# Performance work log

Hardware: AMD Instinct MI355X
Metric: run time of the kernel (lower is better)

The kernel has to match this reference:

```python
import jax, jax.numpy as jnp
import numpy as np

B, N, C_IN, C_OUT = 32, 4096, 16, 64
EMB, LINK, WIN = 16, 3, 12


def setup_inputs() -> dict:
    key = jax.random.key(0)
    ks = jax.random.split(key, 7)
    s = lambda k, shape, sc=1.0: jax.random.normal(k, shape, dtype=jnp.float32) * sc
    return {
        "x": s(ks[0], (B, N, C_IN)),
        "x_window": s(ks[1], (B, WIN, N, C_IN)),
        "node_embeddings": s(ks[2], (N, EMB)),
        "weights_pool": s(ks[3], (EMB, LINK, C_IN, C_OUT), 0.1),
        "weights_window": s(ks[4], (EMB, C_IN, C_OUT), 0.1),
        "bias_pool": s(ks[5], (EMB, C_OUT), 0.1),
        "T": s(ks[6], (WIN,), 0.1),
    }


def reference(x, x_window, node_embeddings, weights_pool, weights_window, bias_pool, T):
    # Adaptive adjacency: softmax over rows of relu(E E^T)   [N, N]
    n = node_embeddings.shape[0]
    supports = jax.nn.softmax(
        jax.nn.relu(node_embeddings @ node_embeddings.T), axis=1)
    # Chebyshev polynomial hops: T0=I, T1=A, Tk = 2*A*T(k-1) - T(k-2)
    support_set = [jnp.eye(n, dtype=supports.dtype), supports]
    for _ in range(2, weights_pool.shape[1]):
        support_set.append(2.0 * (supports @ support_set[-1]) - support_set[-2])
    supports_k = jnp.stack(support_set, axis=0)  # [K, N, N]

    # Per-node weight generation from node embeddings
    weights = jnp.einsum('nd,dkio->nkio', node_embeddings, weights_pool)  # [N,K,Cin,Cout]
    bias = node_embeddings @ bias_pool  # [N, Cout]

    # Multi-hop spatial graph convolution
    x_g = jnp.einsum('knm,bmc->bnkc', supports_k, x)  # [B, N, K, Cin]
    x_gconv = jnp.einsum('bnki,nkio->bno', x_g, weights) + bias  # [B, N, Cout]

    # Temporal window transformation: time-mix with T, per-node weights
    x_w = jnp.einsum('btni,t->bni', x_window, T)  # [B, N, Cin]
    w_win = jnp.einsum('nd,dio->nio', node_embeddings, weights_window)  # [N,Cin,Cout]
    x_wconv = jnp.einsum('bni,nio->bno', x_w, w_win)  # [B, N, Cout]

    return x_gconv + x_wconv
```

## Files before the change

kernel.cpp:

```cpp
#include <hip/hip_runtime.h>
#include <hip/hip_bf16.h>

#define NN 4096
#define BB 32
#define CIN 16
#define COUT 64
#define EMB 16
#define KLINK 3
#define WWIN 12
#define BCIN (BB * CIN)
#define KSPLIT 4
#define KCHUNK (NN / KSPLIT)
#define NT (KCHUNK / 32)

typedef unsigned short ushort_t;
typedef __attribute__((ext_vector_type(8))) short bf16x8;
typedef __attribute__((ext_vector_type(4))) float f32x4;
typedef __attribute__((ext_vector_type(4))) unsigned short us4;
typedef __attribute__((ext_vector_type(8))) unsigned short us8;

static __device__ __forceinline__ ushort_t f2bf(float f) {
  union { float f; unsigned u; } v; v.f = f;
  const unsigned r = v.u + 0x7fffu + ((v.u >> 16) & 1u);
  return (ushort_t)(r >> 16);
}

__device__ __forceinline__ void gload16(const void* g, void* l) {
  __builtin_amdgcn_global_load_lds(
      (const __attribute__((address_space(1))) void*)g,
      (__attribute__((address_space(3))) void*)l, 16, 0, 0);
}

__global__ __launch_bounds__(256) void prep_kernel(
    const float* __restrict__ E, const float* __restrict__ Wp,
    const float* __restrict__ Wwp, const float* __restrict__ biasp,
    ushort_t* __restrict__ Ebf, ushort_t* __restrict__ Wpct,
    float* __restrict__ biasn, float* __restrict__ r) {
  const int gid = blockIdx.x * 256 + threadIdx.x;
  if (gid < NN) {
    r[gid] = 0.0f;
    const float* e = E + (size_t)gid * EMB;
    ushort_t* o = Ebf + (size_t)gid * 32;
    #pragma unroll
    for (int d = 0; d < 16; ++d) o[d] = f2bf(e[d]);
    #pragma unroll
    for (int d = 16; d < 32; ++d) o[d] = 0;
  } else if (gid < 2 * NN) {
    const int j = gid - NN;
    const int oo = j >> 6;
    const int i = j & 63;
    const int q = i >> 4;
    const int ii = i & 15;
    ushort_t* w = Wpct + (size_t)j * 32;
    #pragma unroll
    for (int d = 0; d < 16; ++d) {
      float v;
      if (q == 0)
        v = Wp[((size_t)(d * 3 + 0) * 16 + ii) * 64 + oo] -
            Wp[((size_t)(d * 3 + 2) * 16 + ii) * 64 + oo];
      else if (q == 1)
        v = Wp[((size_t)(d * 3 + 1) * 16 + ii) * 64 + oo];
      else if (q == 2)
        v = 2.0f * Wp[((size_t)(d * 3 + 2) * 16 + ii) * 64 + oo];
      else
        v = Wwp[((size_t)d * 16 + ii) * 64 + oo];
      w[d] = f2bf(v);
    }
    #pragma unroll
    for (int d = 16; d < 32; ++d) w[d] = 0;
  } else {
    const int t = gid - 2 * NN;
    if (t < NN * 16) {
      const int n = t >> 4;
      const int o4 = t & 15;
      const float4* bp4 = reinterpret_cast<const float4*>(biasp);
      float4 acc = make_float4(0.f, 0.f, 0.f, 0.f);
      #pragma unroll
      for (int d = 0; d < 16; ++d) {
        const float e = E[(size_t)n * EMB + d];
        const float4 b = bp4[d * 16 + o4];
        acc.x += e * b.x; acc.y += e * b.y; acc.z += e * b.z; acc.w += e * b.w;
      }
      *reinterpret_cast<float4*>(biasn + (size_t)n * 64 + o4 * 4) = acc;
    }
  }
}

__global__ __launch_bounds__(256) void mix_kernel(
    const float* __restrict__ x, const float* __restrict__ xw,
    const float* __restrict__ Tv,
    ushort_t* __restrict__ XtT, float* __restrict__ XW) {
  __shared__ ushort_t T[16][72];
  const int bid = blockIdx.x;
  const int tid = threadIdx.x;
  if (bid < 1024) {
    const int lin = bid * 256 + tid;
    const int c4 = (lin & 3) << 2;
    const int nn0 = ((lin >> 6) & 127) * 32 + ((lin >> 2) & 15);
    const int b = lin >> 13;
    float tv[WWIN];
    #pragma unroll
    for (int t = 0; t < WWIN; ++t) tv[t] = Tv[t];
    float4 a0 = make_float4(0.f, 0.f, 0.f, 0.f);
    float4 a1 = make_float4(0.f, 0.f, 0.f, 0.f);
    #pragma unroll 3
    for (int t = 0; t < WWIN; ++t) {
      const float4 v0 = *reinterpret_cast<const float4*>(
          xw + (((size_t)b * WWIN + t) * NN + nn0) * CIN + c4);
      const float4 v1 = *reinterpret_cast<const float4*>(
          xw + (((size_t)b * WWIN + t) * NN + nn0 + 16) * CIN + c4);
      a0.x += v0.x * tv[t]; a0.y += v0.y * tv[t];
      a0.z += v0.z * tv[t]; a0.w += v0.w * tv[t];
      a1.x += v1.x * tv[t]; a1.y += v1.y * tv[t];
      a1.z += v1.z * tv[t]; a1.w += v1.w * tv[t];
    }
    *reinterpret_cast<float4*>(XW + ((size_t)b * NN + nn0) * CIN + c4) = a0;
    *reinterpret_cast<float4*>(XW + ((size_t)b * NN + nn0 + 16) * CIN + c4) = a1;
  } else {
    const int bx = bid - 1024;
    const int b = bx >> 6;
    const int m0 = (bx & 63) * 64;
    const int i = tid & 15;
    const int ml = tid >> 4;
    #pragma unroll
    for (int it = 0; it < 4; ++it) {
      const int m = m0 + ml + it * 16;
      T[i][ml + it * 16] = f2bf(x[((size_t)b * NN + m) * CIN + i]);
    }
    __syncthreads();
    if (tid < 128) {
      const int rr = tid >> 3;
      const int c8 = (tid & 7) * 8;
      const us8 v = *reinterpret_cast<const us8*>(&T[rr][c8]);
      *reinterpret_cast<us8*>(&XtT[(size_t)(b * CIN + rr) * NN + m0 + c8]) = v;
    }
  }
}

__global__ __launch_bounds__(256) void gemm_mfma_kernel(
    const ushort_t* __restrict__ Ag, const ushort_t* __restrict__ Bt,
    ushort_t* __restrict__ Ct, int lda, int ldb, int ldc, int Kdim) {
  __shared__ ushort_t As[128 * 32];
  __shared__ ushort_t Bs[64 * 32];
  const int tid = threadIdx.x;
  const int lane = tid & 63;
  const int wid = tid >> 6;
  const int wr = wid >> 1;
  const int wc = wid & 1;
  const int row0 = blockIdx.y * 128;
  const int col0 = blockIdx.x * 64;

  f32x4 acc[4][2];
  #pragma unroll
  for (int i = 0; i < 4; ++i)
    #pragma unroll
    for (int j = 0; j < 2; ++j) acc[i][j] = (f32x4){0.f, 0.f, 0.f, 0.f};

  const int sr = tid >> 2;
  const int scs = (((tid & 3) ^ (sr & 3)) * 8);
  const ushort_t* agp0 = Ag + (size_t)(row0 + sr) * lda + scs;
  const ushort_t* agp1 = Ag + (size_t)(row0 + 64 + sr) * lda + scs;
  const ushort_t* bgp  = Bt + (size_t)(col0 + sr) * ldb + scs;
  ushort_t* asl0 = &As[tid * 8];
  ushort_t* asl1 = &As[2048 + tid * 8];
  ushort_t* bsl  = &Bs[tid * 8];

  const int kq = (lane >> 4) * 8;
  const int fr = lane & 15;

  for (int kb = 0; kb < Kdim; kb += 32) {
    gload16(agp0 + kb, asl0);
    gload16(agp1 + kb, asl1);
    gload16(bgp + kb, bsl);
    __syncthreads();

    bf16x8 af[4], bfr[2];
    #pragma unroll
    for (int i = 0; i < 4; ++i) {
      const int r = wr * 64 + i * 16 + fr;
      af[i] = *reinterpret_cast<const bf16x8*>(&As[r * 32 + (kq ^ ((r & 3) * 8))]);
    }
    #pragma unroll
    for (int j = 0; j < 2; ++j) {
      const int r = wc * 32 + j * 16 + fr;
      bfr[j] = *reinterpret_cast<const bf16x8*>(&Bs[r * 32 + (kq ^ ((r & 3) * 8))]);
    }
    #pragma unroll
    for (int i = 0; i < 4; ++i)
      #pragma unroll
      for (int j = 0; j < 2; ++j)
        acc[i][j] = __builtin_amdgcn_mfma_f32_16x16x32_bf16(af[i], bfr[j],
                                                            acc[i][j], 0, 0, 0);
    __syncthreads();
  }

  #pragma unroll
  for (int i = 0; i < 4; ++i) {
    const int rg = row0 + wr * 64 + i * 16 + ((lane >> 4) << 2);
    #pragma unroll
    for (int j = 0; j < 2; ++j) {
      const int cg = col0 + wc * 32 + j * 16 + (lane & 15);
      us4 o;
      o.x = f2bf(acc[i][j][0]);
      o.y = f2bf(acc[i][j][1]);
      o.z = f2bf(acc[i][j][2]);
      o.w = f2bf(acc[i][j][3]);
      *reinterpret_cast<us4*>(&Ct[(size_t)cg * ldc + rg]) = o;
    }
  }
}

template <int CUR>
__device__ __forceinline__ void compute_tile(
    const ushort_t (&As)[3][128 * 32], const ushort_t (&Bs)[3][64 * 32],
    f32x4 (&acc)[4][2], int wr, int wc, int kq, int fr) {
  bf16x8 af[4], bfr[2];
  #pragma unroll
  for (int i = 0; i < 4; ++i) {
    const int rr = wr * 64 + i * 16 + fr;
    af[i] = *reinterpret_cast<const bf16x8*>(
        &As[CUR][rr * 32 + (kq ^ ((rr & 3) * 8))]);
  }
  #pragma unroll
  for (int j = 0; j < 2; ++j) {
    const int rr = wc * 32 + j * 16 + fr;
    bfr[j] = *reinterpret_cast<const bf16x8*>(
        &Bs[CUR][rr * 32 + (kq ^ ((rr & 3) * 8))]);
  }
  #pragma unroll
  for (int i = 0; i < 4; ++i)
    #pragma unroll
    for (int j = 0; j < 2; ++j)
      acc[i][j] = __builtin_amdgcn_mfma_f32_16x16x32_bf16(af[i], bfr[j],
                                                          acc[i][j], 0, 0, 0);
}

__global__ __launch_bounds__(256) void gemm_splitk_kernel(
    const ushort_t* __restrict__ Ag, const ushort_t* __restrict__ Bt,
    float* __restrict__ Cp, int lda, int ldb, int ldc) {
  __shared__ ushort_t As[3][128 * 32];
  __shared__ ushort_t Bs[3][64 * 32];
  const int tid = threadIdx.x;
  const int lane = tid & 63;
  const int wid = tid >> 6;
  const int wr = wid >> 1;
  const int wc = wid & 1;

  const int gx = gridDim.x, gy = gridDim.y;
  const int nwg = gx * gy * gridDim.z;
  int L = blockIdx.x + gx * (blockIdx.y + gy * blockIdx.z);
  L = (L & 7) * (nwg >> 3) + (L >> 3);
  const int bx = L % gx;
  const int by = (L / gx) % gy;
  const int bz = L / (gx * gy);

  const int row0 = by * 128;
  const int col0 = bx * 64;
  const int kbase = bz * KCHUNK;

  f32x4 acc[4][2];
  #pragma unroll
  for (int i = 0; i < 4; ++i)
    #pragma unroll
    for (int j = 0; j < 2; ++j) acc[i][j] = (f32x4){0.f, 0.f, 0.f, 0.f};

  const int sr = tid >> 2;
  const int scs = (((tid & 3) ^ (sr & 3)) * 8);
  const ushort_t* agp0 = Ag + (size_t)(row0 + sr) * lda + scs;
  const ushort_t* agp1 = Ag + (size_t)(row0 + 64 + sr) * lda + scs;
  const ushort_t* bgp  = Bt + (size_t)(col0 + sr) * ldb + scs;

  const int kq = (lane >> 4) * 8;
  const int fr = lane & 15;

#define STAGE(BUF, KB)                              \
  gload16(agp0 + (KB), &As[BUF][tid * 8]);          \
  gload16(agp1 + (KB), &As[BUF][2048 + tid * 8]);   \
  gload16(bgp + (KB), &Bs[BUF][tid * 8]);

#define PIPE_STEP(CUR, NB, TT)                                  \
  STAGE(NB, kbase + ((TT) + 2) * 32);                           \
  asm volatile("s_waitcnt vmcnt(6)" ::: "memory");              \
  __builtin_amdgcn_s_barrier();                                 \
  __builtin_amdgcn_sched_barrier(0);                            \
  compute_tile<CUR>(As, Bs, acc, wr, wc, kq, fr);               \
  __builtin_amdgcn_sched_barrier(0);                            \
  __builtin_amdgcn_s_barrier();

  STAGE(0, kbase);
  STAGE(1, kbase + 32);

  for (int tt = 0; tt < (NT - 2) / 3; ++tt) {
    const int t3 = tt * 3;
    PIPE_STEP(0, 2, t3 + 0);
    PIPE_STEP(1, 0, t3 + 1);
    PIPE_STEP(2, 1, t3 + 2);
  }
  asm volatile("s_waitcnt vmcnt(3)" ::: "memory");
  __builtin_amdgcn_s_barrier();
  __builtin_amdgcn_sched_barrier(0);
  compute_tile<0>(As, Bs, acc, wr, wc, kq, fr);
  __builtin_amdgcn_sched_barrier(0);
  __builtin_amdgcn_s_barrier();
  asm volatile("s_waitcnt vmcnt(0)" ::: "memory");
  __builtin_amdgcn_s_barrier();
  __builtin_amdgcn_sched_barrier(0);
  compute_tile<1>(As, Bs, acc, wr, wc, kq, fr);

#undef PIPE_STEP
#undef STAGE

  float* cpz = Cp + (size_t)bz * ((size_t)BCIN * NN);
  #pragma unroll
  for (int i = 0; i < 4; ++i) {
    const int rg = row0 + wr * 64 + i * 16 + ((lane >> 4) << 2);
    #pragma unroll
    for (int j = 0; j < 2; ++j) {
      const int cg = col0 + wc * 32 + j * 16 + (lane & 15);
      *reinterpret_cast<f32x4*>(&cpz[(size_t)cg * ldc + rg]) = acc[i][j];
    }
  }
}

__global__ __launch_bounds__(256) void reduce_y1_kernel(
    const float* __restrict__ Cp, const float* __restrict__ R,
    ushort_t* __restrict__ Y1T, ushort_t* __restrict__ Y1n) {
  __shared__ ushort_t T[64][72];
  const int n0 = blockIdx.x * 64;
  const int bc0 = blockIdx.y * 64;
  const int tid = threadIdx.x;
  const size_t SS = (size_t)BCIN * NN;
  #pragma unroll
  for (int q = 0; q < 4; ++q) {
    const int lin = tid + q * 256;
    const int bc = lin >> 4;
    const int nc = (lin & 15) * 4;
    const size_t base = (size_t)(bc0 + bc) * NN + n0 + nc;
    float4 s = *reinterpret_cast<const float4*>(Cp + base);
    #pragma unroll
    for (int z = 1; z < KSPLIT; ++z) {
      const float4 v = *reinterpret_cast<const float4*>(Cp + (size_t)z * SS + base);
      s.x += v.x; s.y += v.y; s.z += v.z; s.w += v.w;
    }
    const float4 rv = *reinterpret_cast<const float4*>(R + n0 + nc);
    us4 o;
    o.x = f2bf(s.x / rv.x); o.y = f2bf(s.y / rv.y);
    o.z = f2bf(s.z / rv.z); o.w = f2bf(s.w / rv.w);
    *reinterpret_cast<us4*>(&Y1T[base]) = o;
    *reinterpret_cast<us4*>(&T[bc][nc]) = o;
  }
  __syncthreads();
  #pragma unroll
  for (int t = 0; t < 2; ++t) {
    const int lin = tid + t * 256;
    const int nr = lin >> 3;
    const int ch = lin & 7;
    us8 v;
    #pragma unroll
    for (int e = 0; e < 8; ++e) v[e] = T[ch * 8 + e][nr];
    *reinterpret_cast<us8*>(&Y1n[(size_t)(n0 + nr) * BCIN + bc0 + ch * 8]) = v;
  }
}

__global__ __launch_bounds__(256) void reduce_y2_kernel(
    const float* __restrict__ Cp, ushort_t* __restrict__ Ct,
    const float* __restrict__ R) {
  const size_t e = ((size_t)blockIdx.x * 256 + threadIdx.x) << 2;
  const size_t SS = (size_t)BCIN * NN;
  float4 s = *reinterpret_cast<const float4*>(Cp + e);
  #pragma unroll
  for (int z = 1; z < KSPLIT; ++z) {
    const float4 v = *reinterpret_cast<const float4*>(Cp + (size_t)z * SS + e);
    s.x += v.x; s.y += v.y; s.z += v.z; s.w += v.w;
  }
  const float ri = 1.0f / R[e >> 9];
  s.x *= ri; s.y *= ri; s.z *= ri; s.w *= ri;
  us4 o;
  o.x = f2bf(s.x); o.y = f2bf(s.y); o.z = f2bf(s.z); o.w = f2bf(s.w);
  *reinterpret_cast<us4*>(Ct + e) = o;
}

__global__ __launch_bounds__(256) void pgemm_kernel(
    const ushort_t* __restrict__ Ebf, ushort_t* __restrict__ Pb,
    float* __restrict__ r) {
  __shared__ ushort_t As[128 * 32];
  __shared__ ushort_t Bs[64 * 32];
  const int tid = threadIdx.x;
  const int lane = tid & 63;
  const int wid = tid >> 6;
  const int wr = wid >> 1;
  const int wc = wid & 1;
  const int row0 = blockIdx.y * 128;
  const int col0 = blockIdx.x * 64;

  const int sr = tid >> 2;
  const int scs = (((tid & 3) ^ (sr & 3)) * 8);
  gload16(Ebf + (size_t)(row0 + sr) * 32 + scs, &As[tid * 8]);
  gload16(Ebf + (size_t)(row0 + 64 + sr) * 32 + scs, &As[2048 + tid * 8]);
  gload16(Ebf + (size_t)(col0 + sr) * 32 + scs, &Bs[tid * 8]);
  __syncthreads();

  const int kq = (lane >> 4) * 8;
  const int fr = lane & 15;
  bf16x8 af[4], bfr[2];
  #pragma unroll
  for (int i = 0; i < 4; ++i) {
    const int rr = wr * 64 + i * 16 + fr;
    af[i] = *reinterpret_cast<const bf16x8*>(&As[rr * 32 + (kq ^ ((rr & 3) * 8))]);
  }
  #pragma unroll
  for (int j = 0; j < 2; ++j) {
    const int rr = wc * 32 + j * 16 + fr;
    bfr[j] = *reinterpret_cast<const bf16x8*>(&Bs[rr * 32 + (kq ^ ((rr & 3) * 8))]);
  }
  f32x4 acc[4][2];
  #pragma unroll
  for (int i = 0; i < 4; ++i)
    #pragma unroll
    for (int j = 0; j < 2; ++j) acc[i][j] = (f32x4){0.f, 0.f, 0.f, 0.f};
  #pragma unroll
  for (int i = 0; i < 4; ++i)
    #pragma unroll
    for (int j = 0; j < 2; ++j)
      acc[i][j] = __builtin_amdgcn_mfma_f32_16x16x32_bf16(af[i], bfr[j],
                                                          acc[i][j], 0, 0, 0);

  float pv[4][2][4];
  #pragma unroll
  for (int i = 0; i < 4; ++i) {
    const int rg = row0 + wr * 64 + i * 16 + ((lane >> 4) << 2);
    #pragma unroll
    for (int j = 0; j < 2; ++j) {
      const int cg = col0 + wc * 32 + j * 16 + (lane & 15);
      us4 o;
      #pragma unroll
      for (int q = 0; q < 4; ++q) {
        const float p = __expf(fmaxf(acc[i][j][q], 0.0f) - 16.0f);
        pv[i][j][q] = p;
        o[q] = f2bf(p);
      }
      *reinterpret_cast<us4*>(&Pb[(size_t)cg * NN + rg]) = o;
    }
  }
  #pragma unroll
  for (int i = 0; i < 4; ++i) {
    const int rg = row0 + wr * 64 + i * 16 + ((lane >> 4) << 2);
    #pragma unroll
    for (int q = 0; q < 4; ++q) {
      float s = pv[i][0][q] + pv[i][1][q];
      s += __shfl_xor(s, 1, 64);
      s += __shfl_xor(s, 2, 64);
      s += __shfl_xor(s, 4, 64);
      s += __shfl_xor(s, 8, 64);
      if ((lane & 15) == 0) atomicAdd(&r[rg + q], s);
    }
  }
}

__global__ __launch_bounds__(256) void combine_kernel(
    const float* __restrict__ x, const ushort_t* __restrict__ Y1n,
    const ushort_t* __restrict__ Y2n, const float* __restrict__ XW,
    const ushort_t* __restrict__ Wall, const float* __restrict__ biasn,
    float* __restrict__ out) {
  __shared__ ushort_t lds[4 * 6144];
  const int tid = threadIdx.x;
  const int lane = tid & 63;
  const int w = tid >> 6;
  ushort_t* Wl = lds + w * 6144;
  ushort_t* Vl = Wl + 4096;

  const int perm = ((lane >> 3) << 3) | ((lane & 7) ^ (lane >> 3));
  const int vb = lane >> 1;
  const int i0 = (lane & 1) * 8;

  for (int it = 0; it < 2; ++it) {
    const int n = blockIdx.x * 8 + w * 2 + it;
    asm volatile("s_waitcnt lgkmcnt(0)" ::: "memory");

    const ushort_t* wrow = Wall + (size_t)n * 4096;
    #pragma unroll
    for (int q = 0; q < 8; ++q)
      gload16(wrow + q * 512 + perm * 8, Wl + q * 512);

    const float4* xp = reinterpret_cast<const float4*>(
        x + ((size_t)vb * NN + n) * CIN + i0);
    const float4 xa = xp[0], xb = xp[1];
    const us8 y1 = *reinterpret_cast<const us8*>(Y1n + (size_t)n * BCIN + lane * 8);
    const us8 y2 = *reinterpret_cast<const us8*>(Y2n + (size_t)n * BCIN + lane * 8);
    const float4* xwp = reinterpret_cast<const float4*>(
        XW + ((size_t)vb * NN + n) * CIN + i0);
    const float4 wa = xwp[0], wb = xwp[1];
    us8 xv, wv;
    xv[0] = f2bf(xa.x); xv[1] = f2bf(xa.y); xv[2] = f2bf(xa.z); xv[3] = f2bf(xa.w);
    xv[4] = f2bf(xb.x); xv[5] = f2bf(xb.y); xv[6] = f2bf(xb.z); xv[7] = f2bf(xb.w);
    wv[0] = f2bf(wa.x); wv[1] = f2bf(wa.y); wv[2] = f2bf(wa.z); wv[3] = f2bf(wa.w);
    wv[4] = f2bf(wb.x); wv[5] = f2bf(wb.y); wv[6] = f2bf(wb.z); wv[7] = f2bf(wb.w);
    const int c0 = (lane & 1);
    const int vswz = vb & 7;
    *reinterpret_cast<us8*>(Vl + vb * 64 + (((c0 + 0) ^ vswz) << 3)) = xv;
    *reinterpret_cast<us8*>(Vl + vb * 64 + (((c0 + 2) ^ vswz) << 3)) = y1;
    *reinterpret_cast<us8*>(Vl + vb * 64 + (((c0 + 4) ^ vswz) << 3)) = y2;
    *reinterpret_cast<us8*>(Vl + vb * 64 + (((c0 + 6) ^ vswz) << 3)) = wv;

    f32x4 acc[2][4];
    #pragma unroll
    for (int nt = 0; nt < 4; ++nt) {
      const float bv = biasn[(size_t)n * 64 + nt * 16 + (lane & 15)];
      acc[0][nt] = (f32x4){bv, bv, bv, bv};
      acc[1][nt] = (f32x4){bv, bv, bv, bv};
    }

    asm volatile("s_waitcnt vmcnt(0)" ::: "memory");

    bf16x8 af[2][2], bfr[4][2];
    #pragma unroll
    for (int mt = 0; mt < 2; ++mt)
      #pragma unroll
      for (int kt = 0; kt < 2; ++kt) {
        const int rr = mt * 16 + (lane & 15);
        const int c = kt * 4 + (lane >> 4);
        af[mt][kt] = *reinterpret_cast<const bf16x8*>(
            Vl + rr * 64 + ((c ^ (lane & 7)) << 3));
      }
    #pragma unroll
    for (int nt = 0; nt < 4; ++nt)
      #pragma unroll
      for (int kt = 0; kt < 2; ++kt) {
        const int o = nt * 16 + (lane & 15);
        const int c = kt * 4 + (lane >> 4);
        bfr[nt][kt] = *reinterpret_cast<const bf16x8*>(
            Wl + o * 64 + ((c ^ (lane & 7)) << 3));
      }
    #pragma unroll
    for (int mt = 0; mt < 2; ++mt)
      #pragma unroll
      for (int nt = 0; nt < 4; ++nt)
        #pragma unroll
        for (int kt = 0; kt < 2; ++kt)
          acc[mt][nt] = __builtin_amdgcn_mfma_f32_16x16x32_bf16(
              af[mt][kt], bfr[nt][kt], acc[mt][nt], 0, 0, 0);

    #pragma unroll
    for (int mt = 0; mt < 2; ++mt)
      #pragma unroll
      for (int nt = 0; nt < 4; ++nt) {
        const int o = nt * 16 + (lane & 15);
        #pragma unroll
        for (int rr = 0; rr < 4; ++rr) {
          const int b = mt * 16 + ((lane >> 4) << 2) + rr;
          out[((size_t)b * NN + n) * COUT + o] = acc[mt][nt][rr];
        }
      }
  }
}

extern "C" void kernel_launch(void* const* d_in, const int* in_sizes, int n_in,
                              void* d_out, int out_size, void* d_ws,
                              size_t ws_size, hipStream_t stream) {
  const float* x = (const float*)d_in[0];
  const float* x_window = (const float*)d_in[1];
  const float* E = (const float*)d_in[2];
  const float* Wp = (const float*)d_in[3];
  const float* Wwp = (const float*)d_in[4];
  const float* biasp = (const float*)d_in[5];
  const float* Tv = (const float*)d_in[6];
  float* out = (float*)d_out;

  char* p = (char*)d_ws;
  float* XW = (float*)p;                 p += (size_t)BB * NN * CIN * 4;
  ushort_t* Pb = (ushort_t*)p;           p += (size_t)NN * NN * 2;
  ushort_t* XtT = (ushort_t*)p;          p += (size_t)BCIN * NN * 2;
  ushort_t* Y1T = (ushort_t*)p;          p += (size_t)BCIN * NN * 2;
  ushort_t* Y2n = (ushort_t*)p;          p += (size_t)NN * BCIN * 2;
  ushort_t* Y1n = (ushort_t*)p;          p += (size_t)NN * BCIN * 2;
  ushort_t* Wall = (ushort_t*)p;         p += (size_t)NN * 4096 * 2;
  ushort_t* Ebf = (ushort_t*)p;          p += (size_t)NN * 32 * 2;
  ushort_t* Wpct = (ushort_t*)p;         p += (size_t)NN * 32 * 2;
  float* biasn = (float*)p;              p += (size_t)NN * 64 * 4;
  float* r = (float*)p;                  p += (size_t)NN * 4;
  float* Cpart = (float*)p;              p += (size_t)KSPLIT * BCIN * NN * 4;

  prep_kernel<<<288, 256, 0, stream>>>(E, Wp, Wwp, biasp, Ebf, Wpct, biasn, r);
  gemm_mfma_kernel<<<dim3(NN / 64, NN / 128), 256, 0, stream>>>(
      Wpct, Ebf, Wall, 32, 32, NN, 32);
  pgemm_kernel<<<dim3(NN / 64, NN / 128), 256, 0, stream>>>(Ebf, Pb, r);
  mix_kernel<<<3072, 256, 0, stream>>>(x, x_window, Tv, XtT, XW);
  gemm_splitk_kernel<<<dim3(BCIN / 64, NN / 128, KSPLIT), 256, 0, stream>>>(
      Pb, XtT, Cpart, NN, NN, NN);
  reduce_y1_kernel<<<dim3(NN / 64, BCIN / 64), 256, 0, stream>>>(
      Cpart, r, Y1T, Y1n);
  gemm_splitk_kernel<<<dim3(NN / 64, BCIN / 128, KSPLIT), 256, 0, stream>>>(
      Y1T, Pb, Cpart, NN, NN, BCIN);
  reduce_y2_kernel<<<(BCIN * NN / 4) / 256, 256, 0, stream>>>(Cpart, Y2n, r);
  combine_kernel<<<NN / 8, 256, 0, stream>>>(x, Y1n, Y2n, XW, Wall, biasn, out);
}
```

Before: 192.8 us.

## Merge weight GEMM, P GEMM and mix kernels into one interleaved launch

Three independent kernels (the per-node weight GEMM, the exp(relu(EE^T)) GEMM with row sums, and the time-mix/transpose kernel) are merged into a single uber_kernel. Work types are interleaved by block index in groups of 14, so compute-heavy MFMA tiles and bandwidth-heavy mix blocks share the GPU at the same time. This removes two launch gaps and the tail-end idling between them. The cost is a larger shared-memory footprint per block, set by the biggest role, which may lower occupancy for the lighter roles.

New measurement: 180.4 us. 6.4% less time.

```diff
diff --git a/kernel.cpp b/kernel.cpp
--- a/kernel.cpp
+++ b/kernel.cpp
@@ -86,15 +86,148 @@
   }
 }
 
-__global__ __launch_bounds__(256) void mix_kernel(
+__global__ __launch_bounds__(256) void uber_kernel(
+    const ushort_t* __restrict__ Ebf, const ushort_t* __restrict__ Wpct,
+    ushort_t* __restrict__ Wall, ushort_t* __restrict__ Pb,
+    float* __restrict__ r,
     const float* __restrict__ x, const float* __restrict__ xw,
     const float* __restrict__ Tv,
     ushort_t* __restrict__ XtT, float* __restrict__ XW) {
-  __shared__ ushort_t T[16][72];
+  __shared__ ushort_t smem[6144];
   const int bid = blockIdx.x;
   const int tid = threadIdx.x;
-  if (bid < 1024) {
-    const int lin = bid * 256 + tid;
+  const int g = bid / 14;
+  const int rm = bid - g * 14;
+
+  if (rm < 4) {
+    const int pidx = g * 4 + rm;
+    const int row0 = (pidx >> 6) * 128;
+    const int col0 = (pidx & 63) * 64;
+    ushort_t* As = smem;
+    ushort_t* Bs = smem + 4096;
+    const int lane = tid & 63;
+    const int wid = tid >> 6;
+    const int wr = wid >> 1;
+    const int wc = wid & 1;
+    const int sr = tid >> 2;
+    const int scs = (((tid & 3) ^ (sr & 3)) * 8);
+    gload16(Ebf + (size_t)(row0 + sr) * 32 + scs, &As[tid * 8]);
+    gload16(Ebf + (size_t)(row0 + 64 + sr) * 32 + scs, &As[2048 + tid * 8]);
+    gload16(Ebf + (size_t)(col0 + sr) * 32 + scs, &Bs[tid * 8]);
+    __syncthreads();
+
+    const int kq = (lane >> 4) * 8;
+    const int fr = lane & 15;
+    bf16x8 af[4], bfr[2];
+    #pragma unroll
+    for (int i = 0; i < 4; ++i) {
+      const int rr = wr * 64 + i * 16 + fr;
+      af[i] = *reinterpret_cast<const bf16x8*>(&As[rr * 32 + (kq ^ ((rr & 3) * 8))]);
+    }
+    #pragma unroll
+    for (int j = 0; j < 2; ++j) {
+      const int rr = wc * 32 + j * 16 + fr;
+      bfr[j] = *reinterpret_cast<const bf16x8*>(&Bs[rr * 32 + (kq ^ ((rr & 3) * 8))]);
+    }
+    f32x4 acc[4][2];
+    #pragma unroll
+    for (int i = 0; i < 4; ++i)
+      #pragma unroll
+      for (int j = 0; j < 2; ++j) acc[i][j] = (f32x4){0.f, 0.f, 0.f, 0.f};
+    #pragma unroll
+    for (int i = 0; i < 4; ++i)
+      #pragma unroll
+      for (int j = 0; j < 2; ++j)
+        acc[i][j] = __builtin_amdgcn_mfma_f32_16x16x32_bf16(af[i], bfr[j],
+                                                            acc[i][j], 0, 0, 0);
+    float pv[4][2][4];
+    #pragma unroll
+    for (int i = 0; i < 4; ++i) {
+      const int rg = row0 + wr * 64 + i * 16 + ((lane >> 4) << 2);
+      #pragma unroll
+      for (int j = 0; j < 2; ++j) {
+        const int cg = col0 + wc * 32 + j * 16 + (lane & 15);
+        us4 o;
+        #pragma unroll
+        for (int q = 0; q < 4; ++q) {
+          const float p = __expf(fmaxf(acc[i][j][q], 0.0f) - 16.0f);
+          pv[i][j][q] = p;
+          o[q] = f2bf(p);
+        }
+        *reinterpret_cast<us4*>(&Pb[(size_t)cg * NN + rg]) = o;
+      }
+    }
+    #pragma unroll
+    for (int i = 0; i < 4; ++i) {
+      const int rg = row0 + wr * 64 + i * 16 + ((lane >> 4) << 2);
+      #pragma unroll
+      for (int q = 0; q < 4; ++q) {
+        float s = pv[i][0][q] + pv[i][1][q];
+        s += __shfl_xor(s, 1, 64);
+        s += __shfl_xor(s, 2, 64);
+        s += __shfl_xor(s, 4, 64);
+        s += __shfl_xor(s, 8, 64);
+        if ((lane & 15) == 0) atomicAdd(&r[rg + q], s);
+      }
+    }
+  } else if (rm < 8) {
+    const int widx = g * 4 + (rm - 4);
+    const int row0 = (widx >> 6) * 128;
+    const int col0 = (widx & 63) * 64;
+    ushort_t* As = smem;
+    ushort_t* Bs = smem + 4096;
+    const int lane = tid & 63;
+    const int wid = tid >> 6;
+    const int wr = wid >> 1;
+    const int wc = wid & 1;
+    const int sr = tid >> 2;
+    const int scs = (((tid & 3) ^ (sr & 3)) * 8);
+    gload16(Wpct + (size_t)(row0 + sr) * 32 + scs, &As[tid * 8]);
+    gload16(Wpct + (size_t)(row0 + 64 + sr) * 32 + scs, &As[2048 + tid * 8]);
+    gload16(Ebf + (size_t)(col0 + sr) * 32 + scs, &Bs[tid * 8]);
+    __syncthreads();
+
+    const int kq = (lane >> 4) * 8;
+    const int fr = lane & 15;
+    bf16x8 af[4], bfr[2];
+    #pragma unroll
+    for (int i = 0; i < 4; ++i) {
+      const int rr = wr * 64 + i * 16 + fr;
+      af[i] = *reinterpret_cast<const bf16x8*>(&As[rr * 32 + (kq ^ ((rr & 3) * 8))]);
+    }
+    #pragma unroll
+    for (int j = 0; j < 2; ++j) {
+      const int rr = wc * 32 + j * 16 + fr;
+      bfr[j] = *reinterpret_cast<const bf16x8*>(&Bs[rr * 32 + (kq ^ ((rr & 3) * 8))]);
+    }
+    f32x4 acc[4][2];
+    #pragma unroll
+    for (int i = 0; i < 4; ++i)
+      #pragma unroll
+      for (int j = 0; j < 2; ++j) acc[i][j] = (f32x4){0.f, 0.f, 0.f, 0.f};
+    #pragma unroll
+    for (int i = 0; i < 4; ++i)
+      #pragma unroll
+      for (int j = 0; j < 2; ++j)
+        acc[i][j] = __builtin_amdgcn_mfma_f32_16x16x32_bf16(af[i], bfr[j],
+                                                            acc[i][j], 0, 0, 0);
+    #pragma unroll
+    for (int i = 0; i < 4; ++i) {
+      const int rg = row0 + wr * 64 + i * 16 + ((lane >> 4) << 2);
+      #pragma unroll
+      for (int j = 0; j < 2; ++j) {
+        const int cg = col0 + wc * 32 + j * 16 + (lane & 15);
+        us4 o;
+        o.x = f2bf(acc[i][j][0]);
+        o.y = f2bf(acc[i][j][1]);
+        o.z = f2bf(acc[i][j][2]);
+        o.w = f2bf(acc[i][j][3]);
+        *reinterpret_cast<us4*>(&Wall[(size_t)cg * NN + rg]) = o;
+      }
+    }
+  } else if (rm < 10) {
+    const int tidx = g * 2 + (rm - 8);
+    const int lin = tidx * 256 + tid;
     const int c4 = (lin & 3) << 2;
     const int nn0 = ((lin >> 6) & 127) * 32 + ((lin >> 2) & 15);
     const int b = lin >> 13;
@@ -117,9 +250,10 @@
     *reinterpret_cast<float4*>(XW + ((size_t)b * NN + nn0) * CIN + c4) = a0;
     *reinterpret_cast<float4*>(XW + ((size_t)b * NN + nn0 + 16) * CIN + c4) = a1;
   } else {
-    const int bx = bid - 1024;
-    const int b = bx >> 6;
-    const int m0 = (bx & 63) * 64;
+    const int txidx = g * 4 + (rm - 10);
+    const int b = txidx >> 6;
+    const int m0 = (txidx & 63) * 64;
+    ushort_t (*T)[72] = reinterpret_cast<ushort_t(*)[72]>(smem);
     const int i = tid & 15;
     const int ml = tid >> 4;
     #pragma unroll
@@ -133,79 +267,6 @@
       const int c8 = (tid & 7) * 8;
       const us8 v = *reinterpret_cast<const us8*>(&T[rr][c8]);
       *reinterpret_cast<us8*>(&XtT[(size_t)(b * CIN + rr) * NN + m0 + c8]) = v;
-    }
-  }
-}
-
-__global__ __launch_bounds__(256) void gemm_mfma_kernel(
-    const ushort_t* __restrict__ Ag, const ushort_t* __restrict__ Bt,
-    ushort_t* __restrict__ Ct, int lda, int ldb, int ldc, int Kdim) {
-  __shared__ ushort_t As[128 * 32];
-  __shared__ ushort_t Bs[64 * 32];
-  const int tid = threadIdx.x;
-  const int lane = tid & 63;
-  const int wid = tid >> 6;
-  const int wr = wid >> 1;
-  const int wc = wid & 1;
-  const int row0 = blockIdx.y * 128;
-  const int col0 = blockIdx.x * 64;
-
-  f32x4 acc[4][2];
-  #pragma unroll
-  for (int i = 0; i < 4; ++i)
-    #pragma unroll
-    for (int j = 0; j < 2; ++j) acc[i][j] = (f32x4){0.f, 0.f, 0.f, 0.f};
-
-  const int sr = tid >> 2;
-  const int scs = (((tid & 3) ^ (sr & 3)) * 8);
-  const ushort_t* agp0 = Ag + (size_t)(row0 + sr) * lda + scs;
-  const ushort_t* agp1 = Ag + (size_t)(row0 + 64 + sr) * lda + scs;
-  const ushort_t* bgp  = Bt + (size_t)(col0 + sr) * ldb + scs;
-  ushort_t* asl0 = &As[tid * 8];
-  ushort_t* asl1 = &As[2048 + tid * 8];
-  ushort_t* bsl  = &Bs[tid * 8];
-
-  const int kq = (lane >> 4) * 8;
-  const int fr = lane & 15;
-
-  for (int kb = 0; kb < Kdim; kb += 32) {
-    gload16(agp0 + kb, asl0);
-    gload16(agp1 + kb, asl1);
-    gload16(bgp + kb, bsl);
-    __syncthreads();
-
-    bf16x8 af[4], bfr[2];
-    #pragma unroll
-    for (int i = 0; i < 4; ++i) {
-      const int r = wr * 64 + i * 16 + fr;
-      af[i] = *reinterpret_cast<const bf16x8*>(&As[r * 32 + (kq ^ ((r & 3) * 8))]);
-    }
-    #pragma unroll
-    for (int j = 0; j < 2; ++j) {
-      const int r = wc * 32 + j * 16 + fr;
-      bfr[j] = *reinterpret_cast<const bf16x8*>(&Bs[r * 32 + (kq ^ ((r & 3) * 8))]);
-    }
-    #pragma unroll
-    for (int i = 0; i < 4; ++i)
-      #pragma unroll
-      for (int j = 0; j < 2; ++j)
-        acc[i][j] = __builtin_amdgcn_mfma_f32_16x16x32_bf16(af[i], bfr[j],
-                                                            acc[i][j], 0, 0, 0);
-    __syncthreads();
-  }
-
-  #pragma unroll
-  for (int i = 0; i < 4; ++i) {
-    const int rg = row0 + wr * 64 + i * 16 + ((lane >> 4) << 2);
-    #pragma unroll
-    for (int j = 0; j < 2; ++j) {
-      const int cg = col0 + wc * 32 + j * 16 + (lane & 15);
-      us4 o;
-      o.x = f2bf(acc[i][j][0]);
-      o.y = f2bf(acc[i][j][1]);
-      o.z = f2bf(acc[i][j][2]);
-      o.w = f2bf(acc[i][j][3]);
-      *reinterpret_cast<us4*>(&Ct[(size_t)cg * ldc + rg]) = o;
     }
   }
 }
@@ -378,83 +439,6 @@
   us4 o;
   o.x = f2bf(s.x); o.y = f2bf(s.y); o.z = f2bf(s.z); o.w = f2bf(s.w);
   *reinterpret_cast<us4*>(Ct + e) = o;
-}
-
-__global__ __launch_bounds__(256) void pgemm_kernel(
-    const ushort_t* __restrict__ Ebf, ushort_t* __restrict__ Pb,
-    float* __restrict__ r) {
-  __shared__ ushort_t As[128 * 32];
-  __shared__ ushort_t Bs[64 * 32];
-  const int tid = threadIdx.x;
-  const int lane = tid & 63;
-  const int wid = tid >> 6;
-  const int wr = wid >> 1;
-  const int wc = wid & 1;
-  const int row0 = blockIdx.y * 128;
-  const int col0 = blockIdx.x * 64;
-
-  const int sr = tid >> 2;
-  const int scs = (((tid & 3) ^ (sr & 3)) * 8);
-  gload16(Ebf + (size_t)(row0 + sr) * 32 + scs, &As[tid * 8]);
-  gload16(Ebf + (size_t)(row0 + 64 + sr) * 32 + scs, &As[2048 + tid * 8]);
-  gload16(Ebf + (size_t)(col0 + sr) * 32 + scs, &Bs[tid * 8]);
-  __syncthreads();
-
-  const int kq = (lane >> 4) * 8;
-  const int fr = lane & 15;
-  bf16x8 af[4], bfr[2];
-  #pragma unroll
-  for (int i = 0; i < 4; ++i) {
-    const int rr = wr * 64 + i * 16 + fr;
-    af[i] = *reinterpret_cast<const bf16x8*>(&As[rr * 32 + (kq ^ ((rr & 3) * 8))]);
-  }
-  #pragma unroll
-  for (int j = 0; j < 2; ++j) {
-    const int rr = wc * 32 + j * 16 + fr;
-    bfr[j] = *reinterpret_cast<const bf16x8*>(&Bs[rr * 32 + (kq ^ ((rr & 3) * 8))]);
-  }
-  f32x4 acc[4][2];
-  #pragma unroll
-  for (int i = 0; i < 4; ++i)
-    #pragma unroll
-    for (int j = 0; j < 2; ++j) acc[i][j] = (f32x4){0.f, 0.f, 0.f, 0.f};
-  #pragma unroll
-  for (int i = 0; i < 4; ++i)
-    #pragma unroll
-    for (int j = 0; j < 2; ++j)
-      acc[i][j] = __builtin_amdgcn_mfma_f32_16x16x32_bf16(af[i], bfr[j],
-                                                          acc[i][j], 0, 0, 0);
-
-  float pv[4][2][4];
-  #pragma unroll
-  for (int i = 0; i < 4; ++i) {
-    const int rg = row0 + wr * 64 + i * 16 + ((lane >> 4) << 2);
-    #pragma unroll
-    for (int j = 0; j < 2; ++j) {
-      const int cg = col0 + wc * 32 + j * 16 + (lane & 15);
-      us4 o;
-      #pragma unroll
-      for (int q = 0; q < 4; ++q) {
-        const float p = __expf(fmaxf(acc[i][j][q], 0.0f) - 16.0f);
-        pv[i][j][q] = p;
-        o[q] = f2bf(p);
-      }
-      *reinterpret_cast<us4*>(&Pb[(size_t)cg * NN + rg]) = o;
-    }
-  }
-  #pragma unroll
-  for (int i = 0; i < 4; ++i) {
-    const int rg = row0 + wr * 64 + i * 16 + ((lane >> 4) << 2);
-    #pragma unroll
-    for (int q = 0; q < 4; ++q) {
-      float s = pv[i][0][q] + pv[i][1][q];
-      s += __shfl_xor(s, 1, 64);
-      s += __shfl_xor(s, 2, 64);
-      s += __shfl_xor(s, 4, 64);
-      s += __shfl_xor(s, 8, 64);
-      if ((lane & 15) == 0) atomicAdd(&r[rg + q], s);
-    }
-  }
 }
 
 __global__ __launch_bounds__(256) void combine_kernel(
@@ -581,10 +565,8 @@
   float* Cpart = (float*)p;              p += (size_t)KSPLIT * BCIN * NN * 4;
 
   prep_kernel<<<288, 256, 0, stream>>>(E, Wp, Wwp, biasp, Ebf, Wpct, biasn, r);
-  gemm_mfma_kernel<<<dim3(NN / 64, NN / 128), 256, 0, stream>>>(
-      Wpct, Ebf, Wall, 32, 32, NN, 32);
-  pgemm_kernel<<<dim3(NN / 64, NN / 128), 256, 0, stream>>>(Ebf, Pb, r);
-  mix_kernel<<<3072, 256, 0, stream>>>(x, x_window, Tv, XtT, XW);
+  uber_kernel<<<7168, 256, 0, stream>>>(Ebf, Wpct, Wall, Pb, r,
+                                        x, x_window, Tv, XtT, XW);
   gemm_splitk_kernel<<<dim3(BCIN / 64, NN / 128, KSPLIT), 256, 0, stream>>>(
       Pb, XtT, Cpart, NN, NN, NN);
   reduce_y1_kernel<<<dim3(NN / 64, BCIN / 64), 256, 0, stream>>>(
```
